# Kernel tuning notes

Measured on AMD Instinct MI355X. Metric: run time of the kernel, lower is better.

Reference implementation:

```python
import jax, jax.numpy as jnp
import numpy as np

B, S, D, H, K = 2, 4096, 256, 8, 32  # batch, seq, d_model, heads, key_dim
LN_EPS = 1e-3  # keras LayerNormalization default epsilon
NEG_INF = -1e9


def setup_inputs() -> dict:
    key = jax.random.key(0)
    ks = jax.random.split(key, 12)
    sd = 1.0 / np.sqrt(D)
    inp = {
        "x": jax.random.normal(ks[0], (B, S, D), dtype=jnp.float32),
        "Wq": jax.random.normal(ks[1], (D, H, K), dtype=jnp.float32) * sd,
        "bq": jnp.zeros((H, K), dtype=jnp.float32),
        "Wk": jax.random.normal(ks[2], (D, H, K), dtype=jnp.float32) * sd,
        "bk": jnp.zeros((H, K), dtype=jnp.float32),
        "Wv": jax.random.normal(ks[3], (D, H, K), dtype=jnp.float32) * sd,
        "bv": jnp.zeros((H, K), dtype=jnp.float32),
        "Wo": jax.random.normal(ks[4], (H, K, D), dtype=jnp.float32) * (1.0 / np.sqrt(H * K)),
        "bo": jnp.zeros((D,), dtype=jnp.float32),
        "gamma": jnp.ones((D,), dtype=jnp.float32),
        "beta": jnp.zeros((D,), dtype=jnp.float32),
        "w_2": 64,
    }
    return inp


def reference(x, Wq, bq, Wk, bk, Wv, bv, Wo, bo, gamma, beta, w_2):
    # q/k/v projections: [B,S,D] -> [B,S,H,K]
    q = jnp.einsum("bsd,dhk->bshk", x, Wq) + bq
    k = jnp.einsum("bsd,dhk->bshk", x, Wk) + bk
    v = jnp.einsum("bsd,dhk->bshk", x, Wv) + bv

    # dense scores (keras MHA computes full L^2 then masks): [B,H,S,S]
    scores = jnp.einsum("bqhk,bshk->bhqs", q, k) / jnp.sqrt(jnp.float32(K))

    # sliding-window band mask |i-j| <= w_2, applied additively like keras
    i = jnp.arange(S)
    band = (jnp.abs(i[:, None] - i[None, :]) <= w_2)  # [S,S]
    scores = scores + (1.0 - band.astype(scores.dtype)) * NEG_INF

    attn = jax.nn.softmax(scores, axis=-1)
    o = jnp.einsum("bhqs,bshk->bqhk", attn, v)
    attn_out = jnp.einsum("bqhk,hkd->bqd", o, Wo) + bo

    # residual add + LayerNorm (last axis)
    y = x + attn_out
    mu = jnp.mean(y, axis=-1, keepdims=True)
    var = jnp.mean(jnp.square(y - mu), axis=-1, keepdims=True)
    return (y - mu) * jax.lax.rsqrt(var + LN_EPS) * gamma + beta
```

## Files before the change

kernel.cpp:

```cpp
#include <hip/hip_runtime.h>
#include <hip/hip_bf16.h>
#include <cmath>

constexpr int B = 2, S = 4096, D = 256, H = 8, K = 32;
constexpr int HK = H * K;
constexpr float LN_EPS = 1e-3f;

constexpr int QT  = 64;
constexpr int WIN = 192;
constexpr int VSTRIDE = 4224;

typedef short bf16x8 __attribute__((ext_vector_type(8)));
typedef float f32x4  __attribute__((ext_vector_type(4)));

static __device__ inline short f2bf(float f) {
    unsigned u = __float_as_uint(f);
    unsigned r = (u + 0x7fffu + ((u >> 16) & 1u)) >> 16;
    return (short)r;
}

static __device__ inline int frag_off(int row, int q) {
    return ((row << 2) + (q ^ ((row >> 1) & 3))) << 4;
}

__global__ __launch_bounds__(256) void wcvt_kernel(
    const float* __restrict__ Wq, const float* __restrict__ Wk,
    const float* __restrict__ Wv, const float* __restrict__ Wo,
    const float* __restrict__ x,
    short* __restrict__ wqt, short* __restrict__ wkt,
    short* __restrict__ wvt, short* __restrict__ wot,
    short* __restrict__ vtb, short* __restrict__ xb)
{
    const int t = threadIdx.x;
    if (blockIdx.x >= 32) {
        const int i = ((blockIdx.x - 32) * 256 + t) * 8;
        const float4 a = *(const float4*)(x + i);
        const float4 b = *(const float4*)(x + i + 4);
        bf16x8 o;
        o[0] = f2bf(a.x); o[1] = f2bf(a.y); o[2] = f2bf(a.z); o[3] = f2bf(a.w);
        o[4] = f2bf(b.x); o[5] = f2bf(b.y); o[6] = f2bf(b.z); o[7] = f2bf(b.w);
        *(bf16x8*)(xb + i) = o;
        return;
    }
    const int mat = blockIdx.x >> 3, strip = blockIdx.x & 7;
    const int d0 = strip * 32;
    const float* src = (mat == 0) ? Wq : (mat == 1) ? Wk : (mat == 2) ? Wv : Wo;
    short* dst = (mat == 0) ? wqt : (mat == 1) ? wkt : (mat == 2) ? wvt : wot;

    __shared__ float lds[32][257];
    {
        const int row = t >> 3, c0 = (t & 7) * 32;
#pragma unroll
        for (int i = 0; i < 8; ++i) {
            const float4 f = *(const float4*)(src + (size_t)(d0 + row) * 256 + c0 + i * 4);
            lds[row][c0 + i * 4 + 0] = f.x; lds[row][c0 + i * 4 + 1] = f.y;
            lds[row][c0 + i * 4 + 2] = f.z; lds[row][c0 + i * 4 + 3] = f.w;
        }
    }
    __syncthreads();
    short* orow = dst + (size_t)t * 256 + d0;
#pragma unroll
    for (int u = 0; u < 4; ++u) {
        bf16x8 v;
#pragma unroll
        for (int j = 0; j < 8; ++j)
            v[j] = f2bf(lds[u * 8 + j][t]);
        *(bf16x8*)(orow + u * 8) = v;
    }

    {
        const int e0 = (blockIdx.x * 256 + t) * 8;
        const int r = e0 >> 7;
        const int c = e0 & 127;
        const int col = (c < 64) ? c : (VSTRIDE - 128 + c);
        short* p = vtb + (size_t)r * VSTRIDE + col;
#pragma unroll
        for (int j = 0; j < 8; ++j) p[j] = 0;
    }
}

__global__ __launch_bounds__(256) void qkv_gemm_kernel(
    const short* __restrict__ xb,
    const short* __restrict__ wqt, const short* __restrict__ wkt,
    const short* __restrict__ wvt,
    const float* __restrict__ bq, const float* __restrict__ bk,
    const float* __restrict__ bv,
    short* __restrict__ qb, short* __restrict__ kb, short* __restrict__ vtb)
{
    const int nt = blockIdx.x % 6, mt = blockIdx.x / 6;
    const int mat = nt >> 1, n0 = (nt & 1) * 128, m0 = mt * 128;
    const short* wt  = (mat == 0) ? wqt : (mat == 1) ? wkt : wvt;
    const float* bia = (mat == 0) ? bq  : (mat == 1) ? bk  : bv;

    __shared__ alignas(16) char lds[32768];
    char* AsB = lds;
    char* BsB = lds + 16384;

    const int t = threadIdx.x, wave = t >> 6, lane = t & 63;
    const int wm = (wave & 1) * 64, wn = (wave >> 1) * 64;
    const int quad = lane >> 4, l16 = lane & 15;

    const int srow = t >> 1, shalf = t & 1;
    const short* xrow = xb + (size_t)(m0 + srow) * 256 + shalf * 32;
    const short* wrow = wt + (size_t)(n0 + srow) * 256 + shalf * 32;

    f32x4 acc[4][4];
#pragma unroll
    for (int i = 0; i < 4; ++i)
#pragma unroll
        for (int j = 0; j < 4; ++j) acc[i][j] = (f32x4){0.f, 0.f, 0.f, 0.f};

    bf16x8 an[4], bn[4];
#pragma unroll
    for (int u = 0; u < 4; ++u) {
        an[u] = ((const bf16x8*)xrow)[u];
        bn[u] = ((const bf16x8*)wrow)[u];
    }

    for (int kk = 0; kk < 4; ++kk) {
        __syncthreads();
#pragma unroll
        for (int u = 0; u < 4; ++u) {
            *(bf16x8*)(AsB + shalf * 8192 + frag_off(srow, u)) = an[u];
            *(bf16x8*)(BsB + shalf * 8192 + frag_off(srow, u)) = bn[u];
        }
        __syncthreads();
        if (kk < 3) {
            const int kc = (kk + 1) * 64;
#pragma unroll
            for (int u = 0; u < 4; ++u) {
                an[u] = ((const bf16x8*)(xrow + kc))[u];
                bn[u] = ((const bf16x8*)(wrow + kc))[u];
            }
        }
#pragma unroll
        for (int hh = 0; hh < 2; ++hh) {
            bf16x8 af[4], bf[4];
#pragma unroll
            for (int mi = 0; mi < 4; ++mi)
                af[mi] = *(const bf16x8*)(AsB + hh * 8192 + frag_off(wm + mi * 16 + l16, quad));
#pragma unroll
            for (int ni = 0; ni < 4; ++ni)
                bf[ni] = *(const bf16x8*)(BsB + hh * 8192 + frag_off(wn + ni * 16 + l16, quad));
#pragma unroll
            for (int mi = 0; mi < 4; ++mi)
#pragma unroll
                for (int ni = 0; ni < 4; ++ni)
                    acc[mi][ni] = __builtin_amdgcn_mfma_f32_16x16x32_bf16(
                        af[mi], bf[ni], acc[mi][ni], 0, 0, 0);
        }
    }

    if (mat < 2) {
        short* dst = (mat == 0) ? qb : kb;
#pragma unroll
        for (int ni = 0; ni < 4; ++ni) {
            const int gn = n0 + wn + ni * 16 + l16;
            const float bb = bia[gn];
            const int h = gn >> 5, k2 = gn & 31;
#pragma unroll
            for (int mi = 0; mi < 4; ++mi)
#pragma unroll
                for (int r = 0; r < 4; ++r) {
                    const int gm = m0 + wm + mi * 16 + quad * 4 + r;
                    const int b = gm >> 12, s = gm & 4095;
                    dst[(((size_t)(b * 8 + h)) * 4096 + s) * 32 + k2] = f2bf(acc[mi][ni][r] + bb);
                }
        }
    } else {
#pragma unroll
        for (int ni = 0; ni < 4; ++ni) {
            const int gn = n0 + wn + ni * 16 + l16;
            const float bb = bia[gn];
            const int h = gn >> 5, k2 = gn & 31;
#pragma unroll
            for (int mi = 0; mi < 4; ++mi) {
                const int gm0 = m0 + wm + mi * 16 + quad * 4;
                const int b = gm0 >> 12, s0 = gm0 & 4095;
                short4 pk;
                pk.x = f2bf(acc[mi][ni][0] + bb);
                pk.y = f2bf(acc[mi][ni][1] + bb);
                pk.z = f2bf(acc[mi][ni][2] + bb);
                pk.w = f2bf(acc[mi][ni][3] + bb);
                *(short4*)(vtb + ((size_t)(b * 8 + h) * 32 + k2) * VSTRIDE + 64 + s0) = pk;
            }
        }
    }
}

__global__ __launch_bounds__(256) void attn_kernel(
    const short* __restrict__ qb, const short* __restrict__ kb,
    const short* __restrict__ vtb, short* __restrict__ ob,
    const int* __restrict__ w2p)
{
    const int w2 = *w2p;
    const int bh   = blockIdx.x >> 6;
    const int tile = blockIdx.x & 63;
    const int i0 = tile * QT, jlo = i0 - w2;
    const int t = threadIdx.x, wave = t >> 6, lane = t & 63;
    const int quad = lane >> 4, l16 = lane & 15;

    __shared__ alignas(16) char lds[55808];
    short* Qs  = (short*)lds;
    short* Ks  = (short*)(lds + 4096);
    short* Vts = (short*)(lds + 16384);
    short* Ps  = (short*)(lds + 29184);
    float* redl = (float*)(lds + 54784);

    {
        const int row = t >> 2, unit = t & 3;
        *(bf16x8*)((char*)Qs + frag_off(row, unit)) =
            *(const bf16x8*)(qb + ((size_t)bh * 4096 + i0 + row) * 32 + unit * 8);
    }
#pragma unroll
    for (int it = 0; it < 3; ++it) {
        const int idx = t + it * 256;
        const int row = idx >> 2, unit = idx & 3;
        const int jc = min(max(jlo + row, 0), S - 1);
        *(bf16x8*)((char*)Ks + frag_off(row, unit)) =
            *(const bf16x8*)(kb + ((size_t)bh * 4096 + jc) * 32 + unit * 8);
    }
#pragma unroll
    for (int it = 0; it < 3; ++it) {
        const int idx = t + it * 256;
        const int row = idx / 24, unit = idx % 24;
        *(bf16x8*)(Vts + row * 200 + unit * 8) =
            *(const bf16x8*)(vtb + ((size_t)bh * 32 + row) * VSTRIDE + (jlo + 64) + unit * 8);
    }
    __syncthreads();

    bf16x8 af[4];
#pragma unroll
    for (int mi = 0; mi < 4; ++mi)
        af[mi] = *(const bf16x8*)((char*)Qs + frag_off(mi * 16 + l16, quad));
    f32x4 sc[4][3];
#pragma unroll
    for (int mi = 0; mi < 4; ++mi)
#pragma unroll
        for (int ni = 0; ni < 3; ++ni) sc[mi][ni] = (f32x4){0.f, 0.f, 0.f, 0.f};
#pragma unroll
    for (int ni = 0; ni < 3; ++ni) {
        const bf16x8 bfr = *(const bf16x8*)((char*)Ks + frag_off(wave * 48 + ni * 16 + l16, quad));
#pragma unroll
        for (int mi = 0; mi < 4; ++mi)
            sc[mi][ni] = __builtin_amdgcn_mfma_f32_16x16x32_bf16(af[mi], bfr, sc[mi][ni], 0, 0, 0);
    }

    const float scale = 0.17677669529663687f;
    int colv[3]; bool jok[3];
#pragma unroll
    for (int ni = 0; ni < 3; ++ni) {
        colv[ni] = wave * 48 + ni * 16 + l16;
        const int j = jlo + colv[ni];
        jok[ni] = (j >= 0) && (j < S);
    }
    float lloc[4][4];
#pragma unroll
    for (int mi = 0; mi < 4; ++mi)
#pragma unroll
        for (int r = 0; r < 4; ++r) {
            const int row = mi * 16 + quad * 4 + r;
            float l = 0.f;
#pragma unroll
            for (int ni = 0; ni < 3; ++ni) {
                const int diff = colv[ni] - row;
                const bool valid = jok[ni] && (diff >= 0) && (diff <= 2 * w2);
                const float p = valid ? __expf(sc[mi][ni][r] * scale) : 0.f;
                l += p;
                Ps[row * 200 + colv[ni]] = f2bf(p);
            }
            lloc[mi][r] = l;
        }
#pragma unroll
    for (int mi = 0; mi < 4; ++mi)
#pragma unroll
        for (int r = 0; r < 4; ++r) {
            float l = lloc[mi][r];
#pragma unroll
            for (int off = 1; off < 16; off <<= 1)
                l += __shfl_xor(l, off);
            lloc[mi][r] = l;
        }
    if (l16 == 0) {
#pragma unroll
        for (int mi = 0; mi < 4; ++mi)
#pragma unroll
            for (int r = 0; r < 4; ++r)
                redl[wave * 64 + mi * 16 + quad * 4 + r] = lloc[mi][r];
    }
    __syncthreads();

    const int orow0 = wave * 16;
    f32x4 oacc[2];
    oacc[0] = (f32x4){0.f, 0.f, 0.f, 0.f};
    oacc[1] = (f32x4){0.f, 0.f, 0.f, 0.f};
#pragma unroll
    for (int kk = 0; kk < 6; ++kk) {
        const bf16x8 pa = *(const bf16x8*)(Ps + (orow0 + l16) * 200 + kk * 32 + quad * 8);
#pragma unroll
        for (int ni = 0; ni < 2; ++ni) {
            const bf16x8 vb = *(const bf16x8*)(Vts + (ni * 16 + l16) * 200 + kk * 32 + quad * 8);
            oacc[ni] = __builtin_amdgcn_mfma_f32_16x16x32_bf16(pa, vb, oacc[ni], 0, 0, 0);
        }
    }

    const int b = bh >> 3, h = bh & 7;
#pragma unroll
    for (int r = 0; r < 4; ++r) {
        const int row = orow0 + quad * 4 + r;
        const float L = redl[row] + redl[64 + row] + redl[128 + row] + redl[192 + row];
        const float Linv = 1.f / L;
        const int s = i0 + row;
#pragma unroll
        for (int ni = 0; ni < 2; ++ni) {
            const int d = ni * 16 + l16;
            ob[((size_t)b * 4096 + s) * 256 + h * 32 + d] = f2bf(oacc[ni][r] * Linv);
        }
    }
}

__global__ __launch_bounds__(256) void out_ln_kernel(
    const short* __restrict__ o, const short* __restrict__ wot,
    const float* __restrict__ x, const float* __restrict__ bo,
    const float* __restrict__ gamma, const float* __restrict__ beta,
    float* __restrict__ out)
{
    __shared__ alignas(16) char lds[32 * 260 * 4];
    char* AsB = lds;
    char* BsB = lds + 2048;

    const int t = threadIdx.x, wave = t >> 6, lane = t & 63;
    const int quad = lane >> 4, l16 = lane & 15;
    const int m0 = blockIdx.x * 32;
    const int wn = wave * 64;

    const int arow = t >> 2, aunit = t & 3;
    const short* brow = wot + (size_t)t * 256;

    f32x4 acc[2][4];
#pragma unroll
    for (int i = 0; i < 2; ++i)
#pragma unroll
        for (int j = 0; j < 4; ++j) acc[i][j] = (f32x4){0.f, 0.f, 0.f, 0.f};

    bf16x8 av, bw[4];
    if (t < 128)
        av = *(const bf16x8*)(o + (size_t)(m0 + arow) * 256 + aunit * 8);
#pragma unroll
    for (int u = 0; u < 4; ++u)
        bw[u] = *(const bf16x8*)(brow + u * 8);

    for (int kk = 0; kk < 8; ++kk) {
        __syncthreads();
        if (t < 128)
            *(bf16x8*)(AsB + frag_off(arow, aunit)) = av;
#pragma unroll
        for (int u = 0; u < 4; ++u)
            *(bf16x8*)(BsB + frag_off(t, u)) = bw[u];
        __syncthreads();

        if (kk < 7) {
            const int kc = (kk + 1) * 32;
            if (t < 128)
                av = *(const bf16x8*)(o + (size_t)(m0 + arow) * 256 + kc + aunit * 8);
#pragma unroll
            for (int u = 0; u < 4; ++u)
                bw[u] = *(const bf16x8*)(brow + kc + u * 8);
        }

        bf16x8 afr[2], bfr[4];
#pragma unroll
        for (int mi = 0; mi < 2; ++mi)
            afr[mi] = *(const bf16x8*)(AsB + frag_off(mi * 16 + l16, quad));
#pragma unroll
        for (int ni = 0; ni < 4; ++ni)
            bfr[ni] = *(const bf16x8*)(BsB + frag_off(wn + ni * 16 + l16, quad));
#pragma unroll
        for (int mi = 0; mi < 2; ++mi)
#pragma unroll
            for (int ni = 0; ni < 4; ++ni)
                acc[mi][ni] = __builtin_amdgcn_mfma_f32_16x16x32_bf16(
                    afr[mi], bfr[ni], acc[mi][ni], 0, 0, 0);
    }

    float bov[4];
#pragma unroll
    for (int ni = 0; ni < 4; ++ni) bov[ni] = bo[wn + ni * 16 + l16];
    __syncthreads();
    float* ys = (float*)lds;
#pragma unroll
    for (int mi = 0; mi < 2; ++mi)
#pragma unroll
        for (int ni = 0; ni < 4; ++ni)
#pragma unroll
            for (int r = 0; r < 4; ++r) {
                const int row = mi * 16 + quad * 4 + r;
                const int col = wn + ni * 16 + l16;
                ys[row * 260 + col] = acc[mi][ni][r] + bov[ni];
            }
    __syncthreads();

    const float4 g4 = *(const float4*)(gamma + lane * 4);
    const float4 b4 = *(const float4*)(beta + lane * 4);
#pragma unroll
    for (int rr = 0; rr < 8; ++rr) {
        const int row = wave * 8 + rr;
        const float4 av2 = *(const float4*)(ys + row * 260 + lane * 4);
        const float4 xv = *(const float4*)(x + (size_t)(m0 + row) * 256 + lane * 4);
        const float y0 = xv.x + av2.x, y1 = xv.y + av2.y, y2 = xv.z + av2.z, y3 = xv.w + av2.w;
        float sum = y0 + y1 + y2 + y3;
        float s2 = y0 * y0 + y1 * y1 + y2 * y2 + y3 * y3;
#pragma unroll
        for (int off = 32; off > 0; off >>= 1) {
            sum += __shfl_xor(sum, off);
            s2 += __shfl_xor(s2, off);
        }
        const float mu = sum * (1.f / 256.f);
        const float rstd = rsqrtf(s2 * (1.f / 256.f) - mu * mu + LN_EPS);
        float4 ov;
        ov.x = (y0 - mu) * rstd * g4.x + b4.x;
        ov.y = (y1 - mu) * rstd * g4.y + b4.y;
        ov.z = (y2 - mu) * rstd * g4.z + b4.z;
        ov.w = (y3 - mu) * rstd * g4.w + b4.w;
        *(float4*)(out + (size_t)(m0 + row) * 256 + lane * 4) = ov;
    }
}

extern "C" void kernel_launch(void* const* d_in, const int* in_sizes, int n_in,
                              void* d_out, int out_size, void* d_ws, size_t ws_size,
                              hipStream_t stream) {
    const float* x     = (const float*)d_in[0];
    const float* Wq    = (const float*)d_in[1];
    const float* bq    = (const float*)d_in[2];
    const float* Wk    = (const float*)d_in[3];
    const float* bk    = (const float*)d_in[4];
    const float* Wv    = (const float*)d_in[5];
    const float* bv    = (const float*)d_in[6];
    const float* Wo    = (const float*)d_in[7];
    const float* bo    = (const float*)d_in[8];
    const float* gamma = (const float*)d_in[9];
    const float* beta  = (const float*)d_in[10];
    const int*   w2p   = (const int*)d_in[11];
    float* out = (float*)d_out;

    const size_t NQ = (size_t)B * H * S * K;
    short* qb  = (short*)d_ws;
    short* kb  = qb + NQ;
    short* vtb = kb + NQ;
    short* ob  = vtb + (size_t)16 * 32 * VSTRIDE;
    short* wqt = ob + NQ;
    short* wkt = wqt + 65536;
    short* wvt = wkt + 65536;
    short* wot = wvt + 65536;
    short* xb  = wot + 65536;

    wcvt_kernel<<<dim3(32 + 1024), dim3(256), 0, stream>>>(
        Wq, Wk, Wv, Wo, x, wqt, wkt, wvt, wot, vtb, xb);

    qkv_gemm_kernel<<<dim3(384), dim3(256), 0, stream>>>(
        xb, wqt, wkt, wvt, bq, bk, bv, qb, kb, vtb);

    attn_kernel<<<dim3(B * H * S / QT), dim3(256), 0, stream>>>(
        qb, kb, vtb, ob, w2p);

    out_ln_kernel<<<dim3(B * S / 32), dim3(256), 0, stream>>>(
        ob, wot, x, bo, gamma, beta, out);
}
```

Before: 120.5 us.

## Load MFMA fragments directly from global memory, dropping LDS staging in GEMMs and attention

The QKV GEMM and the output-projection+LayerNorm kernels no longer stage tiles through shared memory. Each lane loads its MFMA fragments straight from global (bf16) memory, and the tiles are smaller, which doubles the grid sizes. The attention kernel likewise reads Q and K fragments directly from global memory and stores the row-sum reduction in padding inside the P buffer, shrinking LDS use. The aim is to remove LDS round-trips and barriers and raise occupancy. The cost is more redundant global/L2 traffic and uncoalesced fragment loads.

After: 130.4 us. 8.2% more time.

```diff
diff --git a/kernel.cpp b/kernel.cpp
--- a/kernel.cpp
+++ b/kernel.cpp
@@ -17,10 +17,6 @@
     unsigned u = __float_as_uint(f);
     unsigned r = (u + 0x7fffu + ((u >> 16) & 1u)) >> 16;
     return (short)r;
-}
-
-static __device__ inline int frag_off(int row, int q) {
-    return ((row << 2) + (q ^ ((row >> 1) & 3))) << 4;
 }
 
 __global__ __launch_bounds__(256) void wcvt_kernel(
@@ -87,79 +83,50 @@
     const float* __restrict__ bv,
     short* __restrict__ qb, short* __restrict__ kb, short* __restrict__ vtb)
 {
-    const int nt = blockIdx.x % 6, mt = blockIdx.x / 6;
-    const int mat = nt >> 1, n0 = (nt & 1) * 128, m0 = mt * 128;
+    const int nt = blockIdx.x % 12, mt = blockIdx.x / 12;
+    const int mat = nt >> 2, n0 = (nt & 3) * 64, m0 = mt * 128;
     const short* wt  = (mat == 0) ? wqt : (mat == 1) ? wkt : wvt;
     const float* bia = (mat == 0) ? bq  : (mat == 1) ? bk  : bv;
 
-    __shared__ alignas(16) char lds[32768];
-    char* AsB = lds;
-    char* BsB = lds + 16384;
-
     const int t = threadIdx.x, wave = t >> 6, lane = t & 63;
-    const int wm = (wave & 1) * 64, wn = (wave >> 1) * 64;
     const int quad = lane >> 4, l16 = lane & 15;
-
-    const int srow = t >> 1, shalf = t & 1;
-    const short* xrow = xb + (size_t)(m0 + srow) * 256 + shalf * 32;
-    const short* wrow = wt + (size_t)(n0 + srow) * 256 + shalf * 32;
-
-    f32x4 acc[4][4];
-#pragma unroll
-    for (int i = 0; i < 4; ++i)
+    const int wm = wave * 32;
+
+    const short* abase = xb + (size_t)(m0 + wm + l16) * 256 + quad * 8;
+    const short* bbase = wt + (size_t)(n0 + l16) * 256 + quad * 8;
+
+    f32x4 acc[2][4];
+#pragma unroll
+    for (int i = 0; i < 2; ++i)
 #pragma unroll
         for (int j = 0; j < 4; ++j) acc[i][j] = (f32x4){0.f, 0.f, 0.f, 0.f};
 
-    bf16x8 an[4], bn[4];
-#pragma unroll
-    for (int u = 0; u < 4; ++u) {
-        an[u] = ((const bf16x8*)xrow)[u];
-        bn[u] = ((const bf16x8*)wrow)[u];
-    }
-
-    for (int kk = 0; kk < 4; ++kk) {
-        __syncthreads();
-#pragma unroll
-        for (int u = 0; u < 4; ++u) {
-            *(bf16x8*)(AsB + shalf * 8192 + frag_off(srow, u)) = an[u];
-            *(bf16x8*)(BsB + shalf * 8192 + frag_off(srow, u)) = bn[u];
-        }
-        __syncthreads();
-        if (kk < 3) {
-            const int kc = (kk + 1) * 64;
-#pragma unroll
-            for (int u = 0; u < 4; ++u) {
-                an[u] = ((const bf16x8*)(xrow + kc))[u];
-                bn[u] = ((const bf16x8*)(wrow + kc))[u];
-            }
-        }
-#pragma unroll
-        for (int hh = 0; hh < 2; ++hh) {
-            bf16x8 af[4], bf[4];
-#pragma unroll
-            for (int mi = 0; mi < 4; ++mi)
-                af[mi] = *(const bf16x8*)(AsB + hh * 8192 + frag_off(wm + mi * 16 + l16, quad));
+#pragma unroll 2
+    for (int k0 = 0; k0 < 256; k0 += 32) {
+        bf16x8 af[2], bf[4];
+#pragma unroll
+        for (int mi = 0; mi < 2; ++mi)
+            af[mi] = *(const bf16x8*)(abase + (size_t)mi * 16 * 256 + k0);
+#pragma unroll
+        for (int ni = 0; ni < 4; ++ni)
+            bf[ni] = *(const bf16x8*)(bbase + (size_t)ni * 16 * 256 + k0);
+#pragma unroll
+        for (int mi = 0; mi < 2; ++mi)
 #pragma unroll
             for (int ni = 0; ni < 4; ++ni)
-                bf[ni] = *(const bf16x8*)(BsB + hh * 8192 + frag_off(wn + ni * 16 + l16, quad));
-#pragma unroll
-            for (int mi = 0; mi < 4; ++mi)
-#pragma unroll
-                for (int ni = 0; ni < 4; ++ni)
-                    acc[mi][ni] = __builtin_amdgcn_mfma_f32_16x16x32_bf16(
-                        af[mi], bf[ni], acc[mi][ni], 0, 0, 0);
-        }
+                acc[mi][ni] = __builtin_amdgcn_mfma_f32_16x16x32_bf16(
+                    af[mi], bf[ni], acc[mi][ni], 0, 0, 0);
     }
 
     if (mat < 2) {
         short* dst = (mat == 0) ? qb : kb;
 #pragma unroll
         for (int ni = 0; ni < 4; ++ni) {
-            const int gn = n0 + wn + ni * 16 + l16;
+            const int gn = n0 + ni * 16 + l16;
             const float bb = bia[gn];
             const int h = gn >> 5, k2 = gn & 31;
 #pragma unroll
-            for (int mi = 0; mi < 4; ++mi)
+            for (int mi = 0; mi < 2; ++mi)
 #pragma unroll
                 for (int r = 0; r < 4; ++r) {
                     const int gm = m0 + wm + mi * 16 + quad * 4 + r;
@@ -170,11 +137,11 @@
     } else {
 #pragma unroll
         for (int ni = 0; ni < 4; ++ni) {
-            const int gn = n0 + wn + ni * 16 + l16;
+            const int gn = n0 + ni * 16 + l16;
             const float bb = bia[gn];
             const int h = gn >> 5, k2 = gn & 31;
 #pragma unroll
-            for (int mi = 0; mi < 4; ++mi) {
+            for (int mi = 0; mi < 2; ++mi) {
                 const int gm0 = m0 + wm + mi * 16 + quad * 4;
                 const int b = gm0 >> 12, s0 = gm0 & 4095;
                 short4 pk;
@@ -200,26 +167,10 @@
     const int t = threadIdx.x, wave = t >> 6, lane = t & 63;
     const int quad = lane >> 4, l16 = lane & 15;
 
-    __shared__ alignas(16) char lds[55808];
-    short* Qs  = (short*)lds;
-    short* Ks  = (short*)(lds + 4096);
-    short* Vts = (short*)(lds + 16384);
-    short* Ps  = (short*)(lds + 29184);
-    float* redl = (float*)(lds + 54784);
-
-    {
-        const int row = t >> 2, unit = t & 3;
-        *(bf16x8*)((char*)Qs + frag_off(row, unit)) =
-            *(const bf16x8*)(qb + ((size_t)bh * 4096 + i0 + row) * 32 + unit * 8);
-    }
-#pragma unroll
-    for (int it = 0; it < 3; ++it) {
-        const int idx = t + it * 256;
-        const int row = idx >> 2, unit = idx & 3;
-        const int jc = min(max(jlo + row, 0), S - 1);
-        *(bf16x8*)((char*)Ks + frag_off(row, unit)) =
-            *(const bf16x8*)(kb + ((size_t)bh * 4096 + jc) * 32 + unit * 8);
-    }
+    __shared__ alignas(16) char lds[38400];
+    short* Vts = (short*)lds;
+    short* Ps  = (short*)(lds + 12800);
+
 #pragma unroll
     for (int it = 0; it < 3; ++it) {
         const int idx = t + it * 256;
@@ -227,12 +178,12 @@
         *(bf16x8*)(Vts + row * 200 + unit * 8) =
             *(const bf16x8*)(vtb + ((size_t)bh * 32 + row) * VSTRIDE + (jlo + 64) + unit * 8);
     }
-    __syncthreads();
 
     bf16x8 af[4];
 #pragma unroll
     for (int mi = 0; mi < 4; ++mi)
-        af[mi] = *(const bf16x8*)((char*)Qs + frag_off(mi * 16 + l16, quad));
+        af[mi] = *(const bf16x8*)(qb + ((size_t)bh * 4096 + i0 + mi * 16 + l16) * 32 + quad * 8);
+
     f32x4 sc[4][3];
 #pragma unroll
     for (int mi = 0; mi < 4; ++mi)
@@ -240,7 +191,9 @@
         for (int ni = 0; ni < 3; ++ni) sc[mi][ni] = (f32x4){0.f, 0.f, 0.f, 0.f};
 #pragma unroll
     for (int ni = 0; ni < 3; ++ni) {
-        const bf16x8 bfr = *(const bf16x8*)((char*)Ks + frag_off(wave * 48 + ni * 16 + l16, quad));
+        const int krow = wave * 48 + ni * 16 + l16;
+        const int jc = min(max(jlo + krow, 0), S - 1);
+        const bf16x8 bfr = *(const bf16x8*)(kb + ((size_t)bh * 4096 + jc) * 32 + quad * 8);
 #pragma unroll
         for (int mi = 0; mi < 4; ++mi)
             sc[mi][ni] = __builtin_amdgcn_mfma_f32_16x16x32_bf16(af[mi], bfr, sc[mi][ni], 0, 0, 0);
@@ -285,8 +238,10 @@
 #pragma unroll
         for (int mi = 0; mi < 4; ++mi)
 #pragma unroll
-            for (int r = 0; r < 4; ++r)
-                redl[wave * 64 + mi * 16 + quad * 4 + r] = lloc[mi][r];
+            for (int r = 0; r < 4; ++r) {
+                const int row = mi * 16 + quad * 4 + r;
+                ((float*)(Ps + row * 200 + 192))[wave] = lloc[mi][r];
+            }
     }
     __syncthreads();
 
@@ -308,8 +263,8 @@
 #pragma unroll
     for (int r = 0; r < 4; ++r) {
         const int row = orow0 + quad * 4 + r;
-        const float L = redl[row] + redl[64 + row] + redl[128 + row] + redl[192 + row];
-        const float Linv = 1.f / L;
+        const float4 lv = *(const float4*)(Ps + row * 200 + 192);
+        const float Linv = 1.f / (lv.x + lv.y + lv.z + lv.w);
         const int s = i0 + row;
 #pragma unroll
         for (int ni = 0; ni < 2; ++ni) {
@@ -325,89 +280,49 @@
     const float* __restrict__ gamma, const float* __restrict__ beta,
     float* __restrict__ out)
 {
-    __shared__ alignas(16) char lds[32 * 260 * 4];
-    char* AsB = lds;
-    char* BsB = lds + 2048;
+    __shared__ float ys[16][260];
 
     const int t = threadIdx.x, wave = t >> 6, lane = t & 63;
     const int quad = lane >> 4, l16 = lane & 15;
-    const int m0 = blockIdx.x * 32;
+    const int m0 = blockIdx.x * 16;
     const int wn = wave * 64;
 
-    const int arow = t >> 2, aunit = t & 3;
-    const short* brow = wot + (size_t)t * 256;
-
-    f32x4 acc[2][4];
-#pragma unroll
-    for (int i = 0; i < 2; ++i)
-#pragma unroll
-        for (int j = 0; j < 4; ++j) acc[i][j] = (f32x4){0.f, 0.f, 0.f, 0.f};
-
-    bf16x8 av, bw[4];
-    if (t < 128)
-        av = *(const bf16x8*)(o + (size_t)(m0 + arow) * 256 + aunit * 8);
-#pragma unroll
-    for (int u = 0; u < 4; ++u)
-        bw[u] = *(const bf16x8*)(brow + u * 8);
-
-    for (int kk = 0; kk < 8; ++kk) {
-        __syncthreads();
-        if (t < 128)
-            *(bf16x8*)(AsB + frag_off(arow, aunit)) = av;
-#pragma unroll
-        for (int u = 0; u < 4; ++u)
-            *(bf16x8*)(BsB + frag_off(t, u)) = bw[u];
-        __syncthreads();
-
-        if (kk < 7) {
-            const int kc = (kk + 1) * 32;
-            if (t < 128)
-                av = *(const bf16x8*)(o + (size_t)(m0 + arow) * 256 + kc + aunit * 8);
-#pragma unroll
-            for (int u = 0; u < 4; ++u)
-                bw[u] = *(const bf16x8*)(brow + kc + u * 8);
-        }
-
-        bf16x8 afr[2], bfr[4];
-#pragma unroll
-        for (int mi = 0; mi < 2; ++mi)
-            afr[mi] = *(const bf16x8*)(AsB + frag_off(mi * 16 + l16, quad));
+    const short* abase = o   + (size_t)(m0 + l16) * 256 + quad * 8;
+    const short* bbase = wot + (size_t)(wn + l16) * 256 + quad * 8;
+
+    f32x4 acc[4];
+#pragma unroll
+    for (int j = 0; j < 4; ++j) acc[j] = (f32x4){0.f, 0.f, 0.f, 0.f};
+
+#pragma unroll 2
+    for (int k0 = 0; k0 < 256; k0 += 32) {
+        const bf16x8 af = *(const bf16x8*)(abase + k0);
+        bf16x8 bf[4];
 #pragma unroll
         for (int ni = 0; ni < 4; ++ni)
-            bfr[ni] = *(const bf16x8*)(BsB + frag_off(wn + ni * 16 + l16, quad));
-#pragma unroll
-        for (int mi = 0; mi < 2; ++mi)
-#pragma unroll
-            for (int ni = 0; ni < 4; ++ni)
-                acc[mi][ni] = __builtin_amdgcn_mfma_f32_16x16x32_bf16(
-                    afr[mi], bfr[ni], acc[mi][ni], 0, 0, 0);
-    }
-
-    float bov[4];
-#pragma unroll
-    for (int ni = 0; ni < 4; ++ni) bov[ni] = bo[wn + ni * 16 + l16];
-    __syncthreads();
-    float* ys = (float*)lds;
-#pragma unroll
-    for (int mi = 0; mi < 2; ++mi)
+            bf[ni] = *(const bf16x8*)(bbase + (size_t)ni * 16 * 256 + k0);
 #pragma unroll
         for (int ni = 0; ni < 4; ++ni)
-#pragma unroll
-            for (int r = 0; r < 4; ++r) {
-                const int row = mi * 16 + quad * 4 + r;
-                const int col = wn + ni * 16 + l16;
-                ys[row * 260 + col] = acc[mi][ni][r] + bov[ni];
-            }
+            acc[ni] = __builtin_amdgcn_mfma_f32_16x16x32_bf16(af, bf[ni], acc[ni], 0, 0, 0);
+    }
+
+#pragma unroll
+    for (int ni = 0; ni < 4; ++ni) {
+        const float bov = bo[wn + ni * 16 + l16];
+#pragma unroll
+        for (int r = 0; r < 4; ++r)
+            ys[quad * 4 + r][wn + ni * 16 + l16] = acc[ni][r] + bov;
+    }
     __syncthreads();
 
     const float4 g4 = *(const float4*)(gamma + lane * 4);
     const float4 b4 = *(const float4*)(beta + lane * 4);
 #pragma unroll
-    for (int rr = 0; rr < 8; ++rr) {
-        const int row = wave * 8 + rr;
-        const float4 av2 = *(const float4*)(ys + row * 260 + lane * 4);
+    for (int rr = 0; rr < 4; ++rr) {
+        const int row = wave * 4 + rr;
+        const float4 av = *(const float4*)(&ys[row][lane * 4]);
         const float4 xv = *(const float4*)(x + (size_t)(m0 + row) * 256 + lane * 4);
-        const float y0 = xv.x + av2.x, y1 = xv.y + av2.y, y2 = xv.z + av2.z, y3 = xv.w + av2.w;
+        const float y0 = xv.x + av.x, y1 = xv.y + av.y, y2 = xv.z + av.z, y3 = xv.w + av.w;
         float sum = y0 + y1 + y2 + y3;
         float s2 = y0 * y0 + y1 * y1 + y2 * y2 + y3 * y3;
 #pragma unroll
@@ -457,12 +372,12 @@
     wcvt_kernel<<<dim3(32 + 1024), dim3(256), 0, stream>>>(
         Wq, Wk, Wv, Wo, x, wqt, wkt, wvt, wot, vtb, xb);
 
-    qkv_gemm_kernel<<<dim3(384), dim3(256), 0, stream>>>(
+    qkv_gemm_kernel<<<dim3(768), dim3(256), 0, stream>>>(
         xb, wqt, wkt, wvt, bq, bk, bv, qb, kb, vtb);
 
     attn_kernel<<<dim3(B * H * S / QT), dim3(256), 0, stream>>>(
         qb, kb, vtb, ob, w2p);
 
-    out_ln_kernel<<<dim3(B * S / 32), dim3(256), 0, stream>>>(
+    out_ln_kernel<<<dim3(B * S / 16), dim3(256), 0, stream>>>(
         ob, wot, x, bo, gamma, beta, out);
 }
```
